# Optimization experiments

Hardware: AMD Instinct MI355X
Metric: run time of the kernel (lower is better)

## Reference

```python
import jax, jax.numpy as jnp
import numpy as np

B, S, D, H = 4, 2048, 1024, 16
HD = D // H  # head dim = 64


def setup_inputs() -> dict:
    key = jax.random.key(0)
    ks = jax.random.split(key, 6)
    hidden_states = jax.random.normal(ks[0], (B, S, D), dtype=jnp.float32)
    attention_mask = jnp.zeros((B, S), dtype=bool)  # ignored by the module (set to None in forward)
    # RoPE cache: standard rotary angles per position
    inv_freq = 1.0 / (10000.0 ** (jnp.arange(0, HD, 2, dtype=jnp.float32) / HD))  # [HD/2]
    ang = jnp.arange(S, dtype=jnp.float32)[:, None] * inv_freq[None, :]  # [S, HD/2]
    ang = jnp.concatenate([ang, ang], axis=-1)  # [S, HD]
    rope_cos = jnp.cos(ang)
    rope_sin = jnp.sin(ang)
    scale = 1.0 / np.sqrt(D)
    Wq = jax.random.normal(ks[1], (D, D), dtype=jnp.float32) * scale
    Wk = jax.random.normal(ks[2], (D, D), dtype=jnp.float32) * scale
    Wv = jax.random.normal(ks[3], (D, D), dtype=jnp.float32) * scale
    return {"hidden_states": hidden_states, "attention_mask": attention_mask,
            "rope_cos": rope_cos, "rope_sin": rope_sin, "Wq": Wq, "Wk": Wk, "Wv": Wv}


def _rotate_half(x):
    x1, x2 = jnp.split(x, 2, axis=-1)
    return jnp.concatenate([-x2, x1], axis=-1)


def _apply_rope(x, cos, sin):
    # x: [B, H, S, HD]; cos/sin: [S, HD]
    return x * cos[None, None, :, :] + _rotate_half(x) * sin[None, None, :, :]


def reference(hidden_states, attention_mask, rope_cos, rope_sin, Wq, Wk, Wv):
    del attention_mask  # forward() sets attention_mask = None
    b, s, d = hidden_states.shape
    # QKV projections (nn.Linear: y = x @ W.T), split into heads -> [B, H, S, HD]
    def proj(W):
        y = jnp.einsum('bsd,ed->bse', hidden_states, W)
        return y.reshape(b, s, H, HD).transpose(0, 2, 1, 3)
    q = _apply_rope(proj(Wq), rope_cos, rope_sin)
    k = _apply_rope(proj(Wk), rope_cos, rope_sin)
    v = proj(Wv)
    # Softmax attention (non-causal, dropout_p=0)
    scores = jnp.einsum('bhqd,bhkd->bhqk', q, k) / np.sqrt(HD)
    probs = jax.nn.softmax(scores, axis=-1)
    ctx = jnp.einsum('bhqk,bhkd->bhqd', probs, v)
    # [B, H, S, HD] -> [B, S, D]
    return ctx.transpose(0, 2, 1, 3).reshape(b, s, d)
```

## Files before the change

### kernel.cpp

```cpp
#include <hip/hip_runtime.h>
#include <hip/hip_bf16.h>
#include <stdint.h>


typedef __attribute__((ext_vector_type(4)))  float    f32x4;
typedef __attribute__((ext_vector_type(16))) float    f32x16;
typedef __attribute__((ext_vector_type(8)))  __bf16   bf16x8;
typedef __attribute__((ext_vector_type(8)))  unsigned short ushort8;
typedef __attribute__((ext_vector_type(4)))  unsigned short ushort4v;
typedef __attribute__((ext_vector_type(4)))  uint32_t uint32x4;
typedef __attribute__((ext_vector_type(2)))  uint32_t uint32x2;

#define QSCALE 0.18033688011112042f
#define SMAX   16.0f

#define GL16(g, l)                                                            \
  __builtin_amdgcn_global_load_lds(                                           \
      (const __attribute__((address_space(1))) void*)(g),                     \
      (__attribute__((address_space(3))) void*)(l), 16, 0, 0)

__device__ inline unsigned short bf(float f) {
  return __builtin_bit_cast(unsigned short, (__bf16)f);
}
__device__ inline uint32_t cvtpk(float lo, float hi) {
  uint32_t r;
  asm volatile("v_cvt_pk_bf16_f32 %0, %1, %2" : "=v"(r) : "v"(lo), "v"(hi));
  return r;
}

__global__ __launch_bounds__(256) void cvt_bf16(
    const float* __restrict__ X,
    const float* __restrict__ Wq, const float* __restrict__ Wk,
    const float* __restrict__ Wv,
    unsigned short* __restrict__ Xb, unsigned short* __restrict__ Wb)
{
  const int seg = blockIdx.y;
  const float* __restrict__ src = (seg == 0) ? X : (seg == 1) ? Wq : (seg == 2) ? Wk : Wv;
  unsigned short* __restrict__ dst = (seg == 0) ? Xb : Wb + (size_t)(seg - 1) * 1048576;
  const size_t n8 = (seg == 0) ? (size_t)1048576 : (size_t)131072;
  const size_t stride = (size_t)gridDim.x * 256;
  for (size_t i = blockIdx.x * 256 + threadIdx.x; i < n8; i += stride) {
    const float4 a = *reinterpret_cast<const float4*>(src + i * 8);
    const float4 b = *reinterpret_cast<const float4*>(src + i * 8 + 4);
    ushort8 o = { bf(a.x), bf(a.y), bf(a.z), bf(a.w), bf(b.x), bf(b.y), bf(b.z), bf(b.w) };
    *reinterpret_cast<ushort8*>(dst + i * 8) = o;
  }
}

__global__ __launch_bounds__(256) void qkv_gemm(
    const unsigned short* __restrict__ Xb, const unsigned short* __restrict__ Wb,
    const float* __restrict__ rc, const float* __restrict__ rs,
    unsigned short* __restrict__ Qb, unsigned short* __restrict__ Kb,
    unsigned short* __restrict__ VbT, int col0, int nheads_c, int gx)
{
  const int nwg = gridDim.x;
  const int q8 = nwg >> 3;
  int w = (blockIdx.x % 8) * q8 + blockIdx.x / 8;
  const int z = w / (gx * 64);
  const int r = w - z * gx * 64;
  const int brow = (r / gx) * 128;
  const int bcol = (r % gx) * 128;

  const unsigned short* __restrict__ Wz = Wb + (size_t)z * 1048576;

  const int tid  = threadIdx.x;
  const int lane = tid & 63;
  const int wid  = tid >> 6;
  const int wm = wid >> 1, wn = wid & 1;
  const int col16 = lane & 15, rowg = lane >> 4;

  __shared__ unsigned short As[128 * 32];
  __shared__ unsigned short Bs[128 * 32];

  f32x4 acc[4][4];
  #pragma unroll
  for (int m = 0; m < 4; ++m)
    #pragma unroll
    for (int n = 0; n < 4; ++n) acc[m][n] = (f32x4)0.f;

  const int srow = wid * 16 + (lane >> 2);
  const int scol = (lane & 3) * 8;
  const unsigned short* gA0 = Xb + (size_t)(brow + srow) * 1024 + scol;
  const unsigned short* gA1 = gA0 + (size_t)64 * 1024;
  const unsigned short* gB0 = Wz + (size_t)(col0 + bcol + srow) * 1024 + scol;
  const unsigned short* gB1 = gB0 + (size_t)64 * 1024;
  unsigned short* lA0 = &As[wid * 16 * 32];
  unsigned short* lA1 = &As[(64 + wid * 16) * 32];
  unsigned short* lB0 = &Bs[wid * 16 * 32];
  unsigned short* lB1 = &Bs[(64 + wid * 16) * 32];

  for (int k0 = 0; k0 < 1024; k0 += 32) {
    GL16(gA0 + k0, lA0);
    GL16(gA1 + k0, lA1);
    GL16(gB0 + k0, lB0);
    GL16(gB1 + k0, lB1);
    __syncthreads();

    bf16x8 af[4], bfv[4];
    #pragma unroll
    for (int m = 0; m < 4; ++m)
      af[m] = __builtin_bit_cast(bf16x8, *reinterpret_cast<const ushort8*>(
                &As[(wm * 64 + m * 16 + col16) * 32 + rowg * 8]));
    #pragma unroll
    for (int n = 0; n < 4; ++n)
      bfv[n] = __builtin_bit_cast(bf16x8, *reinterpret_cast<const ushort8*>(
                &Bs[(wn * 64 + n * 16 + col16) * 32 + rowg * 8]));
    #pragma unroll
    for (int m = 0; m < 4; ++m)
      #pragma unroll
      for (int n = 0; n < 4; ++n)
        acc[m][n] = __builtin_amdgcn_mfma_f32_16x16x32_bf16(af[m], bfv[n], acc[m][n], 0, 0, 0);
    __syncthreads();
  }

  #pragma unroll
  for (int m = 0; m < 4; ++m) {
    #pragma unroll
    for (int n = 0; n < 4; ++n) {
      const int e  = bcol + wn * 64 + n * 16 + col16;
      const int hl = e >> 6, hd = e & 63;
      if (z == 2) {
        const int row0 = brow + wm * 64 + m * 16 + rowg * 4;
        const int b = row0 >> 11, s0 = row0 & 2047;
        ushort4v o = { bf(acc[m][n][0]), bf(acc[m][n][1]), bf(acc[m][n][2]), bf(acc[m][n][3]) };
        *reinterpret_cast<ushort4v*>(
            VbT + ((size_t)(b * nheads_c + hl) * 64 + hd) * 2048 + s0) = o;
      } else {
        unsigned short* __restrict__ outp = (z == 0) ? Qb : Kb;
        #pragma unroll
        for (int j = 0; j < 4; ++j) {
          const int row = brow + wm * 64 + m * 16 + rowg * 4 + j;
          const int b = row >> 11, s = row & 2047;
          const float rot = (n < 2) ? -acc[m][n + 2][j] : acc[m][n - 2][j];
          float v = acc[m][n][j] * rc[s * 64 + hd] + rot * rs[s * 64 + hd];
          if (z == 0) v *= QSCALE;
          outp[((size_t)(b * nheads_c + hl) * 2048 + s) * 64 + hd] = bf(v);
        }
      }
    }
  }
}

__global__ __launch_bounds__(256) void attn(
    const unsigned short* __restrict__ Qb, const unsigned short* __restrict__ Kb,
    const unsigned short* __restrict__ VbT, float* __restrict__ out,
    int col0, int nheads_c)
{
  const int tid = threadIdx.x, lane = tid & 63, wq = tid >> 6;
  const int l31 = lane & 31, hi = lane >> 5;

  int wg = blockIdx.x;
  const int qx = (int)gridDim.x >> 3;
  wg = (wg & 7) * qx + (wg >> 3);
  const int bh = wg >> 4;
  const int q0 = (wg & 15) * 128;
  const int b = bh / nheads_c, hl = bh - b * nheads_c;
  const int hg = (col0 >> 6) + hl;
  const size_t base = (size_t)bh * 2048 * 64;

  __shared__ unsigned short Ks[64 * 72];
  __shared__ unsigned short Vt[64 * 72];
  __shared__ float Ls[4 * 32];

  const int qrow = q0 + wq * 32 + l31;
  bf16x8 qf[4];
  #pragma unroll
  for (int ds = 0; ds < 4; ++ds)
    qf[ds] = __builtin_bit_cast(bf16x8, *reinterpret_cast<const ushort8*>(
        Qb + base + (size_t)qrow * 64 + ds * 16 + hi * 8));

  f32x16 acc0 = (f32x16)0.f, acc1 = (f32x16)0.f;
  float ps = 0.f;

  const int sr = tid >> 3, sc8 = (tid & 7) * 8;

  for (int kt = 0; kt < 32; ++kt) {
    const int key0 = kt * 64;
    {
      ushort8 k0v = *reinterpret_cast<const ushort8*>(Kb + base + (size_t)(key0 + sr) * 64 + sc8);
      ushort8 k1v = *reinterpret_cast<const ushort8*>(Kb + base + (size_t)(key0 + 32 + sr) * 64 + sc8);
      ushort8 v0v = *reinterpret_cast<const ushort8*>(VbT + base + (size_t)sr * 2048 + key0 + sc8);
      ushort8 v1v = *reinterpret_cast<const ushort8*>(VbT + base + (size_t)(32 + sr) * 2048 + key0 + sc8);
      *reinterpret_cast<ushort8*>(&Ks[sr * 72 + sc8]) = k0v;
      *reinterpret_cast<ushort8*>(&Ks[(32 + sr) * 72 + sc8]) = k1v;
      *reinterpret_cast<ushort8*>(&Vt[sr * 72 + sc8]) = v0v;
      *reinterpret_cast<ushort8*>(&Vt[(32 + sr) * 72 + sc8]) = v1v;
    }
    __syncthreads();

    bf16x8 pa[4];
    #pragma unroll
    for (int kb = 0; kb < 2; ++kb) {
      f32x16 s = (f32x16)0.f;
      #pragma unroll
      for (int ds = 0; ds < 4; ++ds) {
        bf16x8 af = __builtin_bit_cast(bf16x8, *reinterpret_cast<const ushort8*>(
            &Ks[(kb * 32 + l31) * 72 + ds * 16 + hi * 8]));
        s = __builtin_amdgcn_mfma_f32_32x32x16_bf16(af, qf[ds], s, 0, 0, 0);
      }
      float p[16];
      #pragma unroll
      for (int rg = 0; rg < 16; ++rg) {
        p[rg] = __builtin_exp2f(s[rg] - SMAX);
        ps += p[rg];
      }
      #pragma unroll
      for (int hf2 = 0; hf2 < 2; ++hf2) {
        uint32_t w0 = cvtpk(p[hf2 * 8 + 0], p[hf2 * 8 + 1]);
        uint32_t w1 = cvtpk(p[hf2 * 8 + 2], p[hf2 * 8 + 3]);
        uint32_t w2 = cvtpk(p[hf2 * 8 + 4], p[hf2 * 8 + 5]);
        uint32_t w3 = cvtpk(p[hf2 * 8 + 6], p[hf2 * 8 + 7]);
        uint32x2 a02 = __builtin_amdgcn_permlane32_swap(w0, w2, false, false);
        uint32x2 a13 = __builtin_amdgcn_permlane32_swap(w1, w3, false, false);
        uint32x4 d4 = { a02[0], a13[0], a02[1], a13[1] };
        pa[kb * 2 + hf2] = __builtin_bit_cast(bf16x8, d4);
      }
    }

    #pragma unroll
    for (int ks = 0; ks < 4; ++ks) {
      bf16x8 vf0 = __builtin_bit_cast(bf16x8, *reinterpret_cast<const ushort8*>(
          &Vt[l31 * 72 + ks * 16 + hi * 8]));
      bf16x8 vf1 = __builtin_bit_cast(bf16x8, *reinterpret_cast<const ushort8*>(
          &Vt[(32 + l31) * 72 + ks * 16 + hi * 8]));
      acc0 = __builtin_amdgcn_mfma_f32_32x32x16_bf16(pa[ks], vf0, acc0, 0, 0, 0);
      acc1 = __builtin_amdgcn_mfma_f32_32x32x16_bf16(pa[ks], vf1, acc1, 0, 0, 0);
    }
    __syncthreads();
  }

  ps += __shfl_xor(ps, 32);
  if (hi == 0) Ls[wq * 32 + l31] = ps;
  #pragma unroll
  for (int rg = 0; rg < 16; ++rg) {
    const int qr = (rg & 3) + 8 * (rg >> 2) + 4 * hi;
    const float inv = 1.0f / Ls[wq * 32 + qr];
    const int s = q0 + wq * 32 + qr;
    float* o = out + ((size_t)(b * 2048 + s)) * 1024 + hg * 64 + l31;
    o[0]  = acc0[rg] * inv;
    o[32] = acc1[rg] * inv;
  }
}

extern "C" void kernel_launch(void* const* d_in, const int* in_sizes, int n_in,
                              void* d_out, int out_size, void* d_ws, size_t ws_size,
                              hipStream_t stream) {
  (void)in_sizes; (void)n_in; (void)out_size;
  const float* X  = (const float*)d_in[0];
  const float* rc = (const float*)d_in[2];
  const float* rs = (const float*)d_in[3];
  const float* Wq = (const float*)d_in[4];
  const float* Wk = (const float*)d_in[5];
  const float* Wv = (const float*)d_in[6];
  float* out = (float*)d_out;

  const size_t fixed = (size_t)2 * 8192 * 1024 + (size_t)3 * 2 * 1024 * 1024;
  int NC = 8;
  for (int nc = 1; nc <= 8; nc <<= 1) {
    size_t need = (size_t)3 * 2 * 8192 * (1024 / nc) + fixed;
    if (need <= ws_size) { NC = nc; break; }
  }
  const int CW = 1024 / NC;
  const int nheads_c = CW >> 6;
  const int nBH = 4 * nheads_c;
  const int gx = CW / 128;
  const size_t pc = (size_t)8192 * CW;

  unsigned short* Qb  = (unsigned short*)d_ws;
  unsigned short* Kb  = Qb + pc;
  unsigned short* VbT = Kb + pc;
  unsigned short* Xb  = VbT + pc;
  unsigned short* Wb  = Xb + (size_t)8192 * 1024;

  cvt_bf16<<<dim3(512, 4), 256, 0, stream>>>(X, Wq, Wk, Wv, Xb, Wb);

  for (int c = 0; c < NC; ++c) {
    const int col0 = c * CW;
    qkv_gemm<<<dim3(gx * 64 * 3), 256, 0, stream>>>(
        Xb, Wb, rc, rs, Qb, Kb, VbT, col0, nheads_c, gx);
    attn<<<dim3(16 * nBH), 256, 0, stream>>>(
        Qb, Kb, VbT, out, col0, nheads_c);
  }
}
```

Baseline: 202.9 us.

## Load K/V fragments directly from global memory in attention, drop LDS staging

Measured after the change: 311.1 us. 53.3% more time.

```diff
diff --git a/kernel.cpp b/kernel.cpp
--- a/kernel.cpp
+++ b/kernel.cpp
@@ -26,6 +26,9 @@
   uint32_t r;
   asm volatile("v_cvt_pk_bf16_f32 %0, %1, %2" : "=v"(r) : "v"(lo), "v"(hi));
   return r;
+}
+__device__ inline bf16x8 ld16(const unsigned short* p) {
+  return __builtin_bit_cast(bf16x8, *reinterpret_cast<const ushort8*>(p));
 }
 
 __global__ __launch_bounds__(256) void cvt_bf16(
@@ -99,12 +102,10 @@
     bf16x8 af[4], bfv[4];
     #pragma unroll
     for (int m = 0; m < 4; ++m)
-      af[m] = __builtin_bit_cast(bf16x8, *reinterpret_cast<const ushort8*>(
-                &As[(wm * 64 + m * 16 + col16) * 32 + rowg * 8]));
+      af[m] = ld16(&As[(wm * 64 + m * 16 + col16) * 32 + rowg * 8]);
     #pragma unroll
     for (int n = 0; n < 4; ++n)
-      bfv[n] = __builtin_bit_cast(bf16x8, *reinterpret_cast<const ushort8*>(
-                &Bs[(wn * 64 + n * 16 + col16) * 32 + rowg * 8]));
+      bfv[n] = ld16(&Bs[(wn * 64 + n * 16 + col16) * 32 + rowg * 8]);
     #pragma unroll
     for (int m = 0; m < 4; ++m)
       #pragma unroll
@@ -158,35 +159,22 @@
   const int hg = (col0 >> 6) + hl;
   const size_t base = (size_t)bh * 2048 * 64;
 
-  __shared__ unsigned short Ks[64 * 72];
-  __shared__ unsigned short Vt[64 * 72];
   __shared__ float Ls[4 * 32];
 
   const int qrow = q0 + wq * 32 + l31;
   bf16x8 qf[4];
   #pragma unroll
   for (int ds = 0; ds < 4; ++ds)
-    qf[ds] = __builtin_bit_cast(bf16x8, *reinterpret_cast<const ushort8*>(
-        Qb + base + (size_t)qrow * 64 + ds * 16 + hi * 8));
+    qf[ds] = ld16(Qb + base + (size_t)qrow * 64 + ds * 16 + hi * 8);
+
+  const unsigned short* Kp0 = Kb  + base + (size_t)l31 * 64 + hi * 8;
+  const unsigned short* Vp0 = VbT + base + (size_t)l31 * 2048 + hi * 8;
 
   f32x16 acc0 = (f32x16)0.f, acc1 = (f32x16)0.f;
   float ps = 0.f;
 
-  const int sr = tid >> 3, sc8 = (tid & 7) * 8;
-
   for (int kt = 0; kt < 32; ++kt) {
     const int key0 = kt * 64;
-    {
-      ushort8 k0v = *reinterpret_cast<const ushort8*>(Kb + base + (size_t)(key0 + sr) * 64 + sc8);
-      ushort8 k1v = *reinterpret_cast<const ushort8*>(Kb + base + (size_t)(key0 + 32 + sr) * 64 + sc8);
-      ushort8 v0v = *reinterpret_cast<const ushort8*>(VbT + base + (size_t)sr * 2048 + key0 + sc8);
-      ushort8 v1v = *reinterpret_cast<const ushort8*>(VbT + base + (size_t)(32 + sr) * 2048 + key0 + sc8);
-      *reinterpret_cast<ushort8*>(&Ks[sr * 72 + sc8]) = k0v;
-      *reinterpret_cast<ushort8*>(&Ks[(32 + sr) * 72 + sc8]) = k1v;
-      *reinterpret_cast<ushort8*>(&Vt[sr * 72 + sc8]) = v0v;
-      *reinterpret_cast<ushort8*>(&Vt[(32 + sr) * 72 + sc8]) = v1v;
-    }
-    __syncthreads();
 
     bf16x8 pa[4];
     #pragma unroll
@@ -194,8 +182,7 @@
       f32x16 s = (f32x16)0.f;
       #pragma unroll
       for (int ds = 0; ds < 4; ++ds) {
-        bf16x8 af = __builtin_bit_cast(bf16x8, *reinterpret_cast<const ushort8*>(
-            &Ks[(kb * 32 + l31) * 72 + ds * 16 + hi * 8]));
+        bf16x8 af = ld16(Kp0 + (size_t)(key0 + kb * 32) * 64 + ds * 16);
         s = __builtin_amdgcn_mfma_f32_32x32x16_bf16(af, qf[ds], s, 0, 0, 0);
       }
       float p[16];
@@ -219,14 +206,11 @@
 
     #pragma unroll
     for (int ks = 0; ks < 4; ++ks) {
-      bf16x8 vf0 = __builtin_bit_cast(bf16x8, *reinterpret_cast<const ushort8*>(
-          &Vt[l31 * 72 + ks * 16 + hi * 8]));
-      bf16x8 vf1 = __builtin_bit_cast(bf16x8, *reinterpret_cast<const ushort8*>(
-          &Vt[(32 + l31) * 72 + ks * 16 + hi * 8]));
+      bf16x8 vf0 = ld16(Vp0 + key0 + ks * 16);
+      bf16x8 vf1 = ld16(Vp0 + (size_t)32 * 2048 + key0 + ks * 16);
       acc0 = __builtin_amdgcn_mfma_f32_32x32x16_bf16(pa[ks], vf0, acc0, 0, 0, 0);
       acc1 = __builtin_amdgcn_mfma_f32_32x32x16_bf16(pa[ks], vf1, acc1, 0, 0, 0);
     }
-    __syncthreads();
   }
 
   ps += __shfl_xor(ps, 32);
```
